# Kernel optimization log

Hardware: AMD Instinct MI355X
Metric: run time of the kernel (lower is better)

## Reference

```python
import jax, jax.numpy as jnp
import numpy as np

N = 100000      # nodes
E = 1200000     # edges
D = 64          # feature dim
RW = 3          # round_window
L = 2           # num_layers
EPS = -1.0      # GIN init_eps -> (1+eps)*h + neighbor_sum == pure neighbor sum
LN_EPS = 1e-5   # torch LayerNorm default eps


def _ln(x):
    # LayerNorm over feature dim, elementwise_affine=False
    mu = jnp.mean(x, axis=-1, keepdims=True)
    var = jnp.var(x, axis=-1, keepdims=True)
    return (x - mu) * jax.lax.rsqrt(var + LN_EPS)


def _gin(h, src, dst):
    # DGL GINConv(None, 'sum'): (1+eps)*h_dst + sum_{src->dst} h_src
    agg = jax.ops.segment_sum(h[src], dst, num_segments=N)
    return (1.0 + EPS) * h + agg


def setup_inputs() -> dict:
    key = jax.random.key(0)
    k1, k2, k3, k4 = jax.random.split(key, 4)
    feature = jax.random.normal(k1, (N, D), dtype=jnp.float32)
    age = jax.random.randint(k2, (N,), 0, RW)
    src = jax.random.randint(k3, (E,), 0, N)
    dst = jax.random.randint(k4, (E,), 0, N)
    return {"feature": feature, "age": age, "src": src, "dst": dst}


def reference(feature, age, src, dst):
    hn = _ln(feature)  # normalize the (tiled) input features
    # window w keeps nodes with age >= w
    mask = (jnp.arange(RW)[:, None] <= age[None, :]).astype(hn.dtype)  # [RW, N]
    h0 = hn[None, :, :] * mask[:, :, None]  # [RW, N, D]
    windows = []
    for w in range(RW):  # small fixed round_window
        h = h0[w]
        feats = [h]
        for _ in range(L):
            h = jax.nn.relu(_ln(_gin(h, src, dst)))
            feats.append(h)
        windows.append(jnp.concatenate(feats, axis=1))  # [N, (L+1)*D]
    h_self = windows[0]
    # temporal_agg == 'mean_final'
    h_temp = jnp.mean(jnp.stack([windows[0] - windows[i] for i in range(1, RW)]), axis=0)
    return jnp.concatenate([h_self, h_temp], axis=1)  # [N, 2*(L+1)*D]
```

## Files before the change

kernel.cpp:

```cpp
#include <hip/hip_runtime.h>
#include <hip/hip_bf16.h>

constexpr int NN  = 100000;
constexpr int EE  = 1200000;
constexpr int D   = 64;
constexpr int CAP = 64;
constexpr int ZROW = NN;
constexpr float LN_EPS = 1e-5f;
constexpr int NXCD = 8;
constexpr int NPX  = (NN + NXCD - 1) / NXCD;
constexpr int FILL_GRP = 256;
constexpr int FILL_BLOCKS = NXCD * FILL_GRP;

__global__ void fillx_kernel(const int* __restrict__ src, const int* __restrict__ dst,
                             const int* __restrict__ age, int* __restrict__ cnt,
                             int* __restrict__ packed) {
    int bid = blockIdx.x;
    int xcd = bid & 7;
    int grp = bid >> 3;
    int lo = xcd * NPX;
    int hi = min(lo + NPX, NN);
    int per = (EE + FILL_GRP - 1) / FILL_GRP;
    int e0 = grp * per;
    int e1 = min(e0 + per, EE);
    for (int e = e0 + (int)threadIdx.x; e < e1; e += (int)blockDim.x) {
        int d = dst[e];
        if (d >= lo && d < hi) {
            int slot = atomicAdd(&cnt[d], 1);
            if (slot < CAP) {
                int s = src[e];
                packed[(size_t)d * CAP + slot] = s | (age[s] << 17);
            }
        }
    }
}

__device__ __forceinline__ float2 bf22f2(ushort2 u) {
    float2 r;
    r.x = __uint_as_float((unsigned)u.x << 16);
    r.y = __uint_as_float((unsigned)u.y << 16);
    return r;
}

__device__ __forceinline__ ushort2 f2bf2(float2 v) {
    __hip_bfloat16 a = __float2bfloat16(v.x);
    __hip_bfloat16 b = __float2bfloat16(v.y);
    ushort2 u;
    u.x = *(const unsigned short*)&a;
    u.y = *(const unsigned short*)&b;
    return u;
}

__device__ __forceinline__ float2 ln_relu_pair(float2 a, bool relu) {
    float s = a.x + a.y;
    #pragma unroll
    for (int m = 1; m < 32; m <<= 1) s += __shfl_xor(s, m);
    float mu = s * (1.f / 64.f);
    float dx = a.x - mu, dy = a.y - mu;
    float q = dx * dx + dy * dy;
    #pragma unroll
    for (int m = 1; m < 32; m <<= 1) q += __shfl_xor(q, m);
    float rs = rsqrtf(q * (1.f / 64.f) + LN_EPS);
    float2 r;
    r.x = dx * rs;
    r.y = dy * rs;
    if (relu) { r.x = fmaxf(r.x, 0.f); r.y = fmaxf(r.y, 0.f); }
    return r;
}

__global__ void ln_kernel(const float* __restrict__ x, __hip_bfloat16* __restrict__ ybf,
                          __hip_bfloat16* __restrict__ A1bf, int* __restrict__ cnt,
                          int nrows) {
    int gid  = blockIdx.x * blockDim.x + threadIdx.x;
    if (gid < NN) cnt[gid] = 0;
    if (gid < 192) {
        A1bf[(size_t)ZROW * 192 + gid] = __float2bfloat16(0.f);
        if (gid < 64) ybf[(size_t)ZROW * D + gid] = __float2bfloat16(0.f);
    }
    int row  = gid >> 6;
    int lane = gid & 63;
    if (row >= nrows) return;
    size_t i = (size_t)row * D + lane;
    float v = x[i];
    float s = v;
    #pragma unroll
    for (int m = 1; m < 64; m <<= 1) s += __shfl_xor(s, m);
    float mu = s * (1.f / 64.f);
    float d = v - mu;
    float q = d * d;
    #pragma unroll
    for (int m = 1; m < 64; m <<= 1) q += __shfl_xor(q, m);
    float r = d * rsqrtf(q * (1.f / 64.f) + LN_EPS);
    ybf[i] = __float2bfloat16(r);
}

__global__ void gather1_kernel(const __hip_bfloat16* __restrict__ hnbf,
                               const int* __restrict__ cnt,
                               const int* __restrict__ packed,
                               __hip_bfloat16* __restrict__ A1bf,
                               float* __restrict__ out) {
    int gid  = blockIdx.x * blockDim.x + threadIdx.x;
    int node = gid >> 6;
    int lane = gid & 63;
    if (node >= NN) return;
    int sl = lane & 31;
    int h  = lane >> 5;
    int n  = min(cnt[node], CAP);
    int nc4 = (n + 3) >> 2;
    int mc  = max(nc4 - 1, 0);
    const int* pl = packed + (size_t)node * CAP;
    float2 a0 = {0.f, 0.f}, a1 = {0.f, 0.f}, a2 = {0.f, 0.f};

    {
        int c0 = min(h, mc), c1 = min(h + 2, mc);
        int4 pa = *reinterpret_cast<const int4*>(pl + 4 * c0);
        int4 pb = *reinterpret_cast<const int4*>(pl + 4 * c1);
        int pA[4] = {pa.x, pa.y, pa.z, pa.w};
        int pB[4] = {pb.x, pb.y, pb.z, pb.w};
        #pragma unroll
        for (int k = 0; k < 8; ++k) {
            int i  = (k < 4) ? (4 * h + k) : (4 * (h + 2) + (k - 4));
            int pk = (k < 4) ? pA[k] : pB[k - 4];
            int idx = (i < n) ? (pk & 0x1FFFF) : ZROW;
            const ushort2* row = reinterpret_cast<const ushort2*>(
                hnbf + (size_t)idx * D);
            float2 v = bf22f2(row[sl]);
            int g = pk >> 17;
            a0.x += v.x; a0.y += v.y;
            if (g >= 1) { a1.x += v.x; a1.y += v.y; }
            if (g >= 2) { a2.x += v.x; a2.y += v.y; }
        }
    }
    for (int c = 4 + h; c < nc4; c += 2) {
        int4 pc = *reinterpret_cast<const int4*>(pl + 4 * c);
        int pC[4] = {pc.x, pc.y, pc.z, pc.w};
        #pragma unroll
        for (int k = 0; k < 4; ++k) {
            int i = 4 * c + k;
            int idx = (i < n) ? (pC[k] & 0x1FFFF) : ZROW;
            const ushort2* row = reinterpret_cast<const ushort2*>(
                hnbf + (size_t)idx * D);
            float2 v = bf22f2(row[sl]);
            int g = pC[k] >> 17;
            a0.x += v.x; a0.y += v.y;
            if (g >= 1) { a1.x += v.x; a1.y += v.y; }
            if (g >= 2) { a2.x += v.x; a2.y += v.y; }
        }
    }
    a0.x += __shfl_xor(a0.x, 32); a0.y += __shfl_xor(a0.y, 32);
    a1.x += __shfl_xor(a1.x, 32); a1.y += __shfl_xor(a1.y, 32);
    a2.x += __shfl_xor(a2.x, 32); a2.y += __shfl_xor(a2.y, 32);

    float2 r0 = ln_relu_pair(a0, true);
    float2 r1 = ln_relu_pair(a1, true);
    float2 r2 = ln_relu_pair(a2, true);

    ushort2* rw = reinterpret_cast<ushort2*>(A1bf + (size_t)node * (3 * D));
    float* ob = out + (size_t)node * 384;
    if (h == 0) {
        rw[sl] = f2bf2(r0);
        reinterpret_cast<float2*>(ob + 64)[sl] = r0;
    } else {
        rw[32 + sl] = f2bf2(r1);
        rw[64 + sl] = f2bf2(r2);
        float2 o4;
        o4.x = r0.x - 0.5f * (r1.x + r2.x);
        o4.y = r0.y - 0.5f * (r1.y + r2.y);
        reinterpret_cast<float2*>(ob + 256)[sl] = o4;
    }
}

__global__ void gather2_kernel(const __hip_bfloat16* __restrict__ hnbf,
                               const __hip_bfloat16* __restrict__ A1bf,
                               const int* __restrict__ cnt, const int* __restrict__ packed,
                               const int* __restrict__ age, float* __restrict__ out) {
    int gid  = blockIdx.x * blockDim.x + threadIdx.x;
    int node = gid >> 6;
    int lane = gid & 63;
    if (node >= NN) return;
    int sl = lane & 31;
    int h  = lane >> 5;
    int n  = min(cnt[node], CAP);
    int nc4 = (n + 3) >> 2;
    int mc  = max(nc4 - 1, 0);
    const int* pl = packed + (size_t)node * CAP;
    float2 a0 = {0.f, 0.f}, a1 = {0.f, 0.f}, a2 = {0.f, 0.f};

    {
        int c0 = min(h, mc), c1 = min(h + 2, mc);
        int4 pa = *reinterpret_cast<const int4*>(pl + 4 * c0);
        int4 pb = *reinterpret_cast<const int4*>(pl + 4 * c1);
        int pA[4] = {pa.x, pa.y, pa.z, pa.w};
        int pB[4] = {pb.x, pb.y, pb.z, pb.w};
        #pragma unroll
        for (int k = 0; k < 8; ++k) {
            int i  = (k < 4) ? (4 * h + k) : (4 * (h + 2) + (k - 4));
            int pk = (k < 4) ? pA[k] : pB[k - 4];
            int idx = (i < n) ? (pk & 0x1FFFF) : ZROW;
            const ushort2* row = reinterpret_cast<const ushort2*>(
                A1bf + (size_t)idx * (3 * D));
            float2 v0 = bf22f2(row[sl]);
            float2 v1 = bf22f2(row[32 + sl]);
            float2 v2 = bf22f2(row[64 + sl]);
            a0.x += v0.x; a0.y += v0.y;
            a1.x += v1.x; a1.y += v1.y;
            a2.x += v2.x; a2.y += v2.y;
        }
    }
    for (int c = 4 + h; c < nc4; c += 2) {
        int4 pc = *reinterpret_cast<const int4*>(pl + 4 * c);
        int pC[4] = {pc.x, pc.y, pc.z, pc.w};
        #pragma unroll
        for (int k = 0; k < 4; ++k) {
            int i = 4 * c + k;
            int idx = (i < n) ? (pC[k] & 0x1FFFF) : ZROW;
            const ushort2* row = reinterpret_cast<const ushort2*>(
                A1bf + (size_t)idx * (3 * D));
            float2 v0 = bf22f2(row[sl]);
            float2 v1 = bf22f2(row[32 + sl]);
            float2 v2 = bf22f2(row[64 + sl]);
            a0.x += v0.x; a0.y += v0.y;
            a1.x += v1.x; a1.y += v1.y;
            a2.x += v2.x; a2.y += v2.y;
        }
    }
    a0.x += __shfl_xor(a0.x, 32); a0.y += __shfl_xor(a0.y, 32);
    a1.x += __shfl_xor(a1.x, 32); a1.y += __shfl_xor(a1.y, 32);
    a2.x += __shfl_xor(a2.x, 32); a2.y += __shfl_xor(a2.y, 32);

    float2 h20 = ln_relu_pair(a0, true);
    float2 h21 = ln_relu_pair(a1, true);
    float2 h22 = ln_relu_pair(a2, true);

    float2 hnv = bf22f2(reinterpret_cast<const ushort2*>(
        hnbf + (size_t)node * D)[sl]);
    int ag = age[node];
    float f = 1.f - 0.5f * (float)((ag >= 1) + (ag >= 2));
    float* ob = out + (size_t)node * 384;
    if (h == 0) {
        reinterpret_cast<float2*>(ob)[sl] = hnv;
        reinterpret_cast<float2*>(ob + 128)[sl] = h20;
    } else {
        float2 o3, o5;
        o3.x = hnv.x * f;
        o3.y = hnv.y * f;
        o5.x = h20.x - 0.5f * (h21.x + h22.x);
        o5.y = h20.y - 0.5f * (h21.y + h22.y);
        reinterpret_cast<float2*>(ob + 192)[sl] = o3;
        reinterpret_cast<float2*>(ob + 320)[sl] = o5;
    }
}

extern "C" void kernel_launch(void* const* d_in, const int* in_sizes, int n_in,
                              void* d_out, int out_size, void* d_ws, size_t ws_size,
                              hipStream_t stream) {
    const float* feature = (const float*)d_in[0];
    const int*   age     = (const int*)d_in[1];
    const int*   src     = (const int*)d_in[2];
    const int*   dst     = (const int*)d_in[3];
    float* out = (float*)d_out;

    size_t nd1 = (size_t)(NN + 1) * D;
    __hip_bfloat16* hnbf = (__hip_bfloat16*)d_ws;
    __hip_bfloat16* A1bf = hnbf + nd1;
    int* cnt    = (int*)(A1bf + (size_t)(NN + 1) * 3 * D);
    int* packed = cnt + NN;

    ln_kernel<<<(int)(((size_t)NN * D + 255) / 256), 256, 0, stream>>>(
        feature, hnbf, A1bf, cnt, NN);
    fillx_kernel<<<FILL_BLOCKS, 256, 0, stream>>>(src, dst, age, cnt, packed);
    gather1_kernel<<<(NN * 64 + 255) / 256, 256, 0, stream>>>(hnbf, cnt, packed, A1bf, out);
    gather2_kernel<<<(NN * 64 + 255) / 256, 256, 0, stream>>>(hnbf, A1bf, cnt, packed,
                                                              age, out);
}
```

Baseline: 207.6 us.

## Replace global-atomic bucket fill with LDS histogram, scan, and LDS-slot fill

Swaps the single fill pass, which did one global atomicAdd per edge on cnt, for three passes. First, per-block LDS histograms per XCD node range are written to a table. Second, an exclusive scan over the blocks gives each block its starting offset per node. Third, a fill pass takes slots with LDS atomics. The aim is to move atomic contention out of global memory and drop the cnt zeroing in the LN kernel. In exchange it reads dst twice, adds two launches and uses 12500-entry int LDS arrays per block (50 KB), which limits occupancy.

```diff
diff --git a/kernel.cpp b/kernel.cpp
--- a/kernel.cpp
+++ b/kernel.cpp
@@ -8,28 +8,64 @@
 constexpr int ZROW = NN;
 constexpr float LN_EPS = 1e-5f;
 constexpr int NXCD = 8;
-constexpr int NPX  = (NN + NXCD - 1) / NXCD;
-constexpr int FILL_GRP = 256;
-constexpr int FILL_BLOCKS = NXCD * FILL_GRP;
-
-__global__ void fillx_kernel(const int* __restrict__ src, const int* __restrict__ dst,
-                             const int* __restrict__ age, int* __restrict__ cnt,
-                             int* __restrict__ packed) {
-    int bid = blockIdx.x;
-    int xcd = bid & 7;
-    int grp = bid >> 3;
+constexpr int NPX  = NN / NXCD;
+constexpr int G    = 32;
+constexpr int FB   = NXCD * G;
+constexpr int EPG  = (EE + G - 1) / G;
+constexpr int FTH  = 512;
+
+__global__ __launch_bounds__(FTH) void histA_kernel(const int* __restrict__ dst,
+                                                    unsigned short* __restrict__ Htab) {
+    __shared__ int hist[NPX];
+    int b = blockIdx.x, xcd = b & 7, k = b >> 3;
     int lo = xcd * NPX;
-    int hi = min(lo + NPX, NN);
-    int per = (EE + FILL_GRP - 1) / FILL_GRP;
-    int e0 = grp * per;
-    int e1 = min(e0 + per, EE);
-    for (int e = e0 + (int)threadIdx.x; e < e1; e += (int)blockDim.x) {
-        int d = dst[e];
-        if (d >= lo && d < hi) {
-            int slot = atomicAdd(&cnt[d], 1);
+    for (int i = threadIdx.x; i < NPX; i += FTH) hist[i] = 0;
+    __syncthreads();
+    int e0 = k * EPG, e1 = min(e0 + EPG, EE);
+    for (int e = e0 + (int)threadIdx.x; e < e1; e += FTH) {
+        int d = dst[e] - lo;
+        if ((unsigned)d < (unsigned)NPX) atomicAdd(&hist[d], 1);
+    }
+    __syncthreads();
+    unsigned short* hrow = Htab + (size_t)(xcd * G + k) * NPX;
+    for (int i = threadIdx.x; i < NPX; i += FTH) hrow[i] = (unsigned short)hist[i];
+}
+
+__global__ void hscan_kernel(const unsigned short* __restrict__ Htab,
+                             unsigned short* __restrict__ Btab, int* __restrict__ cnt) {
+    int d = blockIdx.x * blockDim.x + threadIdx.x;
+    if (d >= NN) return;
+    int xcd = d / NPX, dl = d - xcd * NPX;
+    int run = 0;
+    #pragma unroll 8
+    for (int k = 0; k < G; ++k) {
+        size_t idx = (size_t)(xcd * G + k) * NPX + dl;
+        int c = Htab[idx];
+        Btab[idx] = (unsigned short)run;
+        run += c;
+    }
+    cnt[d] = run;
+}
+
+__global__ __launch_bounds__(FTH) void fillB_kernel(const int* __restrict__ src,
+                                                    const int* __restrict__ dst,
+                                                    const int* __restrict__ age,
+                                                    const unsigned short* __restrict__ Btab,
+                                                    int* __restrict__ packed) {
+    __shared__ int cur[NPX];
+    int b = blockIdx.x, xcd = b & 7, k = b >> 3;
+    int lo = xcd * NPX;
+    const unsigned short* brow = Btab + (size_t)(xcd * G + k) * NPX;
+    for (int i = threadIdx.x; i < NPX; i += FTH) cur[i] = brow[i];
+    __syncthreads();
+    int e0 = k * EPG, e1 = min(e0 + EPG, EE);
+    for (int e = e0 + (int)threadIdx.x; e < e1; e += FTH) {
+        int d = dst[e] - lo;
+        if ((unsigned)d < (unsigned)NPX) {
+            int slot = atomicAdd(&cur[d], 1);
             if (slot < CAP) {
                 int s = src[e];
-                packed[(size_t)d * CAP + slot] = s | (age[s] << 17);
+                packed[(size_t)(d + lo) * CAP + slot] = s | (age[s] << 17);
             }
         }
     }
@@ -69,10 +105,8 @@
 }
 
 __global__ void ln_kernel(const float* __restrict__ x, __hip_bfloat16* __restrict__ ybf,
-                          __hip_bfloat16* __restrict__ A1bf, int* __restrict__ cnt,
-                          int nrows) {
+                          __hip_bfloat16* __restrict__ A1bf, int nrows) {
     int gid  = blockIdx.x * blockDim.x + threadIdx.x;
-    if (gid < NN) cnt[gid] = 0;
     if (gid < 192) {
         A1bf[(size_t)ZROW * 192 + gid] = __float2bfloat16(0.f);
         if (gid < 64) ybf[(size_t)ZROW * D + gid] = __float2bfloat16(0.f);
@@ -265,10 +299,14 @@
     __hip_bfloat16* A1bf = hnbf + nd1;
     int* cnt    = (int*)(A1bf + (size_t)(NN + 1) * 3 * D);
     int* packed = cnt + NN;
+    unsigned short* Htab = (unsigned short*)(packed + (size_t)NN * CAP);
+    unsigned short* Btab = Htab + (size_t)NXCD * G * NPX;
 
     ln_kernel<<<(int)(((size_t)NN * D + 255) / 256), 256, 0, stream>>>(
-        feature, hnbf, A1bf, cnt, NN);
-    fillx_kernel<<<FILL_BLOCKS, 256, 0, stream>>>(src, dst, age, cnt, packed);
+        feature, hnbf, A1bf, NN);
+    histA_kernel<<<FB, FTH, 0, stream>>>(dst, Htab);
+    hscan_kernel<<<(NN + 255) / 256, 256, 0, stream>>>(Htab, Btab, cnt);
+    fillB_kernel<<<FB, FTH, 0, stream>>>(src, dst, age, Btab, packed);
     gather1_kernel<<<(NN * 64 + 255) / 256, 256, 0, stream>>>(hnbf, cnt, packed, A1bf, out);
     gather2_kernel<<<(NN * 64 + 255) / 256, 256, 0, stream>>>(hnbf, A1bf, cnt, packed,
                                                               age, out);
```

Result: slower. 244.5 us (+17.8%).
